# Performance work log

Hardware: AMD Instinct MI355X
Metric: run time of the kernel (lower is better)

## Reference

```python
import jax, jax.numpy as jnp
import numpy as np

N_HEAD = 16
MASK_SCALE = 10000.0  # matches torch buffer construction


def setup_inputs() -> dict:
    key = jax.random.key(0)
    k1, k2 = jax.random.split(key)
    B, T, C = 2, 2048, 1024
    x = jax.random.normal(k1, (B, T, C), dtype=jnp.float32)
    # packed q,k projection: nn.Linear(C, 2C, bias=False) -> weight [2C, C]
    W_attn = jax.random.normal(k2, (2 * C, C), dtype=jnp.float32) * 0.02
    alpha = jnp.array(1.0, dtype=jnp.float32)
    beta = jnp.array(0.1, dtype=jnp.float32)
    gamma = jnp.array(0.1, dtype=jnp.float32)
    return {"x": x, "W_attn": W_attn, "alpha": alpha, "beta": beta, "gamma": gamma}


def _shaped_attention(x, W_attn, alpha, beta, gamma):
    B, T, C = x.shape
    H = N_HEAD
    hd = C // H
    # packed projection then split into q, k (use_v=False -> v comes from x)
    qk = jnp.einsum('btc,oc->bto', x, W_attn)  # [B,T,2C]
    q, k = jnp.split(qk, 2, axis=-1)
    q = q.reshape(B, T, H, hd).transpose(0, 2, 1, 3)  # [B,H,T,hd]
    k = k.reshape(B, T, H, hd).transpose(0, 2, 1, 3)
    v = x.reshape(B, T, H, hd).transpose(0, 2, 1, 3)

    scores = jnp.einsum('bhqd,bhkd->bhqk', q, k) * (hd ** -0.5)
    tril = jnp.tril(jnp.ones((T, T), dtype=bool))
    scores = jnp.where(tril, scores, -jnp.inf)
    att = jax.nn.softmax(scores, axis=-1)  # [B,H,T,T]

    # fixed structured masks, built exactly as the torch buffers
    Id = jax.nn.softmax(jnp.eye(T, dtype=jnp.float32) * MASK_SCALE, axis=-1)
    MC = jax.nn.softmax(tril.astype(jnp.float32) * MASK_SCALE, axis=-1)

    shaped = beta * att + alpha * Id[None, None] - gamma * MC[None, None]
    y = jnp.einsum('bhqk,bhkd->bhqd', shaped, v)
    return y.transpose(0, 2, 1, 3).reshape(B, T, C)  # c_proj is Identity


def reference(x, W_attn, alpha, beta, gamma):
    return _shaped_attention(x, W_attn, alpha, beta, gamma)
```

## Files before the change

kernel.cpp:

```cpp
#include <hip/hip_runtime.h>
#include <hip/hip_bf16.h>

typedef __attribute__((ext_vector_type(8))) short bf16x8;
typedef __attribute__((ext_vector_type(4))) float f32x4;
typedef unsigned short u16;

#define B_  2
#define T_  2048
#define C_  1024
#define H_  16
#define HD_ 64

static __device__ __forceinline__ u16 f2bf(float f) {
  unsigned u = __float_as_uint(f);
  u += 0x7fffu + ((u >> 16) & 1u);
  return (u16)(u >> 16);
}

#define NW4 524288
__global__ __launch_bounds__(256) void prep(
    const float* __restrict__ X, const float* __restrict__ W,
    u16* __restrict__ Xb, u16* __restrict__ Wb,
    u16* __restrict__ Vf, float* __restrict__ SubP64)
{
  __shared__ u16 tr[64][65];
  __shared__ float cs[4][64];
  const int blk = blockIdx.x;
  const int tid = threadIdx.x;

  if (blk < 1024) {
    const int kt = blk & 31, bh = blk >> 5;
    const int b = bh >> 4, h = bh & 15;
    const int w = tid >> 6, lane = tid & 63;
    {
      const int row = tid >> 2;
      const int c0  = (tid & 3) * 16;
      const float* xp = X + ((size_t)b * T_ + kt * 64 + row) * C_ + h * 64 + c0;
      float vals[16];
#pragma unroll
      for (int q = 0; q < 4; ++q) {
        float4 v = *(const float4*)(xp + q * 4);
        vals[q * 4 + 0] = v.x; vals[q * 4 + 1] = v.y;
        vals[q * 4 + 2] = v.z; vals[q * 4 + 3] = v.w;
      }
      u16 xb[16];
#pragma unroll
      for (int i = 0; i < 16; ++i) xb[i] = f2bf(vals[i]);
      u16* xq = Xb + ((size_t)(b * T_ + kt * 64 + row)) * C_ + h * 64 + c0;
      *(bf16x8*)xq       = *(const bf16x8*)&xb[0];
      *(bf16x8*)(xq + 8) = *(const bf16x8*)&xb[8];
#pragma unroll
      for (int i = 0; i < 16; ++i) tr[row][c0 + i] = xb[i];
#pragma unroll
      for (int m = 4; m <= 32; m <<= 1)
#pragma unroll
        for (int i = 0; i < 16; ++i) vals[i] += __shfl_xor(vals[i], m);
      if (lane < 4) {
        float* dst = &cs[w][lane * 16];
#pragma unroll
        for (int q = 0; q < 4; ++q) {
          f32x4 s4 = { vals[q * 4 + 0], vals[q * 4 + 1], vals[q * 4 + 2], vals[q * 4 + 3] };
          *(f32x4*)&dst[q * 4] = s4;
        }
      }
    }
    __syncthreads();
    {
      const int quad = (lane >> 4), l16 = lane & 15;
      u16* outb = Vf + ((size_t)bh * 32 + kt) * 4096;
#pragma unroll
      for (int c = 0; c < 2; ++c) {
        u16 tmp[8];
#pragma unroll
        for (int j = 0; j < 8; ++j) tmp[j] = tr[c * 32 + quad * 8 + j][w * 16 + l16];
        *(bf16x8*)&outb[((w * 2 + c) * 64 + lane) * 8] = *(const bf16x8*)tmp;
      }
    }
    if (tid < 64)
      SubP64[(size_t)bh * 2048 + kt * 64 + tid] =
          cs[0][tid] + cs[1][tid] + cs[2][tid] + cs[3][tid];
  } else {
    int i = (blk - 1024) * 256 + tid;
    float4 v = ((const float4*)W)[i];
    ushort4 u = { f2bf(v.x), f2bf(v.y), f2bf(v.z), f2bf(v.w) };
    ((ushort4*)Wb)[i] = u;
  }
}

__global__ __launch_bounds__(256) void gemm_qk(
    const u16* __restrict__ Xb, const u16* __restrict__ Wb,
    u16* __restrict__ Qo, u16* __restrict__ Kf)
{
  __shared__ __align__(16) u16 As[128 * 64];
  __shared__ __align__(16) u16 Bs[128 * 64];

  const int tid  = threadIdx.x;
  const int w    = tid >> 6;
  const int lane = tid & 63;
  const int quad = lane >> 4;
  const int l16  = lane & 15;
  const int m0 = blockIdx.y * 128;
  const int n0 = blockIdx.x * 128;

  const int grow = w * 8 + ((lane >> 3) & 7);
  const int gcol = (lane & 7) * 8;

  f32x4 zero = {0.f, 0.f, 0.f, 0.f};
  f32x4 acc[4][4];
#pragma unroll
  for (int i = 0; i < 4; ++i)
#pragma unroll
    for (int j = 0; j < 4; ++j) acc[i][j] = zero;

  const int wr = (w >> 1) * 64, wc = (w & 1) * 64;

  for (int k0 = 0; k0 < C_; k0 += 64) {
#pragma unroll
    for (int r = 0; r < 4; ++r) {
      const u16* ga = Xb + (size_t)(m0 + grow + r * 32) * C_ + k0 + gcol;
      const u16* gb = Wb + (size_t)(n0 + grow + r * 32) * C_ + k0 + gcol;
      __builtin_amdgcn_global_load_lds(
          (const __attribute__((address_space(1))) void*)ga,
          (__attribute__((address_space(3))) void*)&As[(w * 8 + r * 32) * 64],
          16, 0, 0);
      __builtin_amdgcn_global_load_lds(
          (const __attribute__((address_space(1))) void*)gb,
          (__attribute__((address_space(3))) void*)&Bs[(w * 8 + r * 32) * 64],
          16, 0, 0);
    }
    __syncthreads();
#pragma unroll
    for (int c = 0; c < 2; ++c) {
      bf16x8 af[4], bf[4];
#pragma unroll
      for (int i = 0; i < 4; ++i)
        af[i] = *(const bf16x8*)&As[(wr + i * 16 + l16) * 64 + c * 32 + quad * 8];
#pragma unroll
      for (int j = 0; j < 4; ++j)
        bf[j] = *(const bf16x8*)&Bs[(wc + j * 16 + l16) * 64 + c * 32 + quad * 8];
#pragma unroll
      for (int i = 0; i < 4; ++i)
#pragma unroll
        for (int j = 0; j < 4; ++j)
          acc[i][j] = __builtin_amdgcn_mfma_f32_16x16x32_bf16(af[i], bf[j], acc[i][j], 0, 0, 0);
    }
    __syncthreads();
  }

#pragma unroll
  for (int i = 0; i < 4; ++i) {
    const int t_base = m0 + wr + i * 16;
    const int bidx = t_base >> 11;
    const int kt   = (t_base & 2047) >> 6;
    const int trow = (t_base & 2047) + quad * 4;
#pragma unroll
    for (int j = 0; j < 4; ++j) {
      const int n = n0 + wc + j * 16 + l16;
      if (n < C_) {
        const int hq = n >> 6, d = n & 63;
        u16* qp = Qo + (((size_t)bidx * H_ + hq) * T_ + trow) * HD_ + d;
#pragma unroll
        for (int r = 0; r < 4; ++r) qp[(size_t)r * HD_] = f2bf(0.125f * acc[i][j][r]);
      } else {
        const int nh = n - C_;
        const int hh = nh >> 6, d = nh & 63;
        u16* kp = Kf + (((((size_t)(bidx * H_ + hh) * 32 + kt) * 4 + i) * 2 + (d >> 5)) * 64
                        + ((d >> 3) & 3) * 16 + quad * 4) * 8 + (d & 7);
#pragma unroll
        for (int r = 0; r < 4; ++r) kp[(size_t)r * 8] = f2bf(acc[i][j][r]);
      }
    }
  }
}

__device__ __forceinline__ void load_kv(
    bf16x8 (&kf)[2][4], bf16x8 (&vf)[2][4],
    const u16* __restrict__ kbase, const u16* __restrict__ vbase, int lane)
{
#pragma unroll
  for (int c = 0; c < 2; ++c)
#pragma unroll
    for (int nb = 0; nb < 4; ++nb) {
      kf[c][nb] = *(const bf16x8*)&kbase[((nb * 2 + c) * 64 + lane) * 8];
      vf[c][nb] = *(const bf16x8*)&vbase[((nb * 2 + c) * 64 + lane) * 8];
    }
}

__device__ __forceinline__ void tile_compute(
    const bf16x8 (&qfrag)[2], const bf16x8 (&kf)[2][4], const bf16x8 (&vf)[2][4],
    f32x4 (&acc)[4], f32x4& accl, float (*pb)[68],
    int quad, int l16, int myrow, bool diag, bf16x8 onesf)
{
  f32x4 zero = {0.f, 0.f, 0.f, 0.f};
  f32x4 sfr[4] = {zero, zero, zero, zero};
#pragma unroll
  for (int cc = 0; cc < 2; ++cc)
#pragma unroll
    for (int nb = 0; nb < 4; ++nb)
      sfr[nb] = __builtin_amdgcn_mfma_f32_16x16x32_bf16(qfrag[cc], kf[cc][nb], sfr[nb], 0, 0, 0);

#pragma unroll
  for (int nb = 0; nb < 4; ++nb)
#pragma unroll
    for (int r = 0; r < 4; ++r) {
      float p = __expf(sfr[nb][r]);
      if (diag && (nb * 16 + l16 > myrow + r)) p = 0.f;
      pb[quad * 4 + r][nb * 16 + l16] = p;
    }

#pragma unroll
  for (int cc = 0; cc < 2; ++cc) {
    f32x4 plo = *(const f32x4*)&pb[l16][cc * 32 + quad * 8];
    f32x4 phi = *(const f32x4*)&pb[l16][cc * 32 + quad * 8 + 4];
    union { unsigned u[4]; bf16x8 v; } pk;
    __hip_bfloat162 hh;
    hh = __float22bfloat162_rn(make_float2(plo[0], plo[1])); pk.u[0] = *(unsigned*)&hh;
    hh = __float22bfloat162_rn(make_float2(plo[2], plo[3])); pk.u[1] = *(unsigned*)&hh;
    hh = __float22bfloat162_rn(make_float2(phi[0], phi[1])); pk.u[2] = *(unsigned*)&hh;
    hh = __float22bfloat162_rn(make_float2(phi[2], phi[3])); pk.u[3] = *(unsigned*)&hh;
    accl = __builtin_amdgcn_mfma_f32_16x16x32_bf16(pk.v, onesf, accl, 0, 0, 0);
#pragma unroll
    for (int nb = 0; nb < 4; ++nb)
      acc[nb] = __builtin_amdgcn_mfma_f32_16x16x32_bf16(pk.v, vf[cc][nb], acc[nb], 0, 0, 0);
  }
}

__global__ __launch_bounds__(256) void attn_kernel(
    const u16* __restrict__ Q, const u16* __restrict__ Kf, const u16* __restrict__ Vf,
    const float* __restrict__ SubP64, const float* __restrict__ X, float* __restrict__ out,
    const float* __restrict__ alphap, const float* __restrict__ betap,
    const float* __restrict__ gammap)
{
  __shared__ __align__(16) char smem[19456];

  const int tid  = threadIdx.x;
  const int w    = tid >> 6;
  const int lane = tid & 63;
  const int quad = lane >> 4;
  const int l16  = lane & 15;
  const int qt = 31 - blockIdx.y;
  const int bh = blockIdx.x;
  const int b = bh >> 4, h = bh & 15;

  const u16* kfb = Kf + (size_t)bh * T_ * HD_;
  const u16* vfb = Vf + (size_t)bh * T_ * HD_;

  bf16x8 qfrag[2];
  {
    const u16* qp = Q + ((size_t)bh * T_ + qt * 64 + w * 16 + l16) * HD_ + quad * 8;
    qfrag[0] = *(const bf16x8*)qp;
    qfrag[1] = *(const bf16x8*)(qp + 32);
  }

  bf16x8 onesf;
#pragma unroll
  for (int j = 0; j < 8; ++j) onesf[j] = (short)0x3F80;

  f32x4 zero = {0.f, 0.f, 0.f, 0.f};
  f32x4 acc[4] = {zero, zero, zero, zero};
  f32x4 accl = zero;
  const int myrow = w * 16 + quad * 4;
  float (*pb)[68] = (float(*)[68])((float*)smem + (size_t)w * 16 * 68);

  bf16x8 kA[2][4], vA[2][4], kB[2][4], vB[2][4];
  load_kv(kA, vA, kfb, vfb, lane);
  int kt = 0;
  for (;;) {
    int ktn = (kt + 1 < qt) ? kt + 1 : qt;
    load_kv(kB, vB, kfb + (size_t)ktn * 4096, vfb + (size_t)ktn * 4096, lane);
    tile_compute(qfrag, kA, vA, acc, accl, pb, quad, l16, myrow, kt == qt, onesf);
    if (kt + 1 > qt) break;
    int ktn2 = (kt + 2 < qt) ? kt + 2 : qt;
    load_kv(kA, vA, kfb + (size_t)ktn2 * 4096, vfb + (size_t)ktn2 * 4096, lane);
    tile_compute(qfrag, kB, vB, acc, accl, pb, quad, l16, myrow, kt + 1 == qt, onesf);
    kt += 2;
    if (kt > qt) break;
  }

  __syncthreads();
  float* Xt = (float*)smem;
  float* G  = (float*)(smem + 17408);
  float* GP = (float*)(smem + 18432);

  {
    const int row = tid >> 2, c0 = (tid & 3) * 16;
    const float* xp = X + ((size_t)b * T_ + qt * 64 + row) * C_ + h * 64 + c0;
#pragma unroll
    for (int q = 0; q < 4; ++q) {
      float4 v = *(const float4*)(xp + q * 4);
      Xt[row * 68 + c0 + q * 4 + 0] = v.x;
      Xt[row * 68 + c0 + q * 4 + 1] = v.y;
      Xt[row * 68 + c0 + q * 4 + 2] = v.z;
      Xt[row * 68 + c0 + q * 4 + 3] = v.w;
    }
  }
  {
    float p = 0.f;
    for (int i = w; i < qt; i += 4)
      p += SubP64[(size_t)bh * 2048 + i * 64 + lane];
    GP[w * 64 + lane] = p;
  }
  __syncthreads();
  {
    float g = 0.f;
#pragma unroll
    for (int i = 0; i < 16; ++i) g += Xt[(w * 16 + i) * 68 + lane];
    G[w * 64 + lane] = g;
  }
  __syncthreads();
  {
    const float alpha = *alphap, gamma = *gammap;
    float run = GP[lane] + GP[64 + lane] + GP[128 + lane] + GP[192 + lane];
    for (int g = 0; g < w; ++g) run += G[g * 64 + lane];
    const int tbase = qt * 64 + w * 16;
#pragma unroll
    for (int i = 0; i < 16; ++i) {
      float v = Xt[(w * 16 + i) * 68 + lane];
      run += v;
      Xt[(w * 16 + i) * 68 + lane] =
          alpha * v - gamma * run * __builtin_amdgcn_rcpf((float)(tbase + i + 1));
    }
  }
  __syncthreads();

  const float beta = *betap;
  float rl[4];
#pragma unroll
  for (int r = 0; r < 4; ++r) rl[r] = beta * __builtin_amdgcn_rcpf(accl[r]);
#pragma unroll
  for (int nb = 0; nb < 4; ++nb) {
#pragma unroll
    for (int r = 0; r < 4; ++r) {
      int t = qt * 64 + myrow + r;
      int d = nb * 16 + l16;
      out[((size_t)b * T_ + t) * C_ + h * 64 + d] =
          Xt[(myrow + r) * 68 + d] + rl[r] * acc[nb][r];
    }
  }
}

extern "C" void kernel_launch(void* const* d_in, const int* in_sizes, int n_in,
                              void* d_out, int out_size, void* d_ws, size_t ws_size,
                              hipStream_t stream) {
  const float* x      = (const float*)d_in[0];
  const float* W_attn = (const float*)d_in[1];
  const float* alphap = (const float*)d_in[2];
  const float* betap  = (const float*)d_in[3];
  const float* gammap = (const float*)d_in[4];
  float* out = (float*)d_out;

  char* ws = (char*)d_ws;
  u16*   Qb     = (u16*)(ws);
  u16*   Kfb    = (u16*)(ws + (8ull  << 20));
  u16*   Vfb    = (u16*)(ws + (16ull << 20));
  float* SubP64 = (float*)(ws + (24ull << 20));
  u16*   Xb     = (u16*)(ws + (25ull << 20));
  u16*   Wb     = (u16*)(ws + (33ull << 20));

  prep<<<3072, 256, 0, stream>>>(x, W_attn, Xb, Wb, Vfb, SubP64);
  gemm_qk<<<dim3(16, 32), 256, 0, stream>>>(Xb, Wb, Qb, Kfb);
  attn_kernel<<<dim3(32, 32), 256, 0, stream>>>(Qb, Kfb, Vfb, SubP64, x, out,
                                                alphap, betap, gammap);
}
```

Measured before the change: 151.8 us.

## Fuse fp32-to-bf16 prep into QK GEMM with register double-buffered loads

Removes the separate prep kernel. The GEMM now reads fp32 X and W directly, converts them to bf16 in registers and stores them into LDS, using register double buffering to prefetch the next k-tile. It also emits the V fragment layout and the column sums from the X tile held in LDS, on the block whose k-tile matches its head. Q is written in an MFMA fragment layout so the attention kernel can load it contiguously. This drops a launch and the bf16 round-trip through global memory. In exchange, each GEMM block redundantly re-reads and re-converts fp32 inputs, and the async global_load_lds path is gone.

```diff
diff --git a/kernel.cpp b/kernel.cpp
--- a/kernel.cpp
+++ b/kernel.cpp
@@ -16,80 +16,62 @@
   u += 0x7fffu + ((u >> 16) & 1u);
   return (u16)(u >> 16);
 }
-
-#define NW4 524288
-__global__ __launch_bounds__(256) void prep(
+static __device__ __forceinline__ unsigned pk2(float a, float b) {
+  __hip_bfloat162 hh = __float22bfloat162_rn(make_float2(a, b));
+  return *(unsigned*)&hh;
+}
+
+__device__ __forceinline__ void mfma_step(
+    const u16* As, const u16* Bs, f32x4 (&acc)[4][4],
+    int wr, int wc, int quad, int l16)
+{
+#pragma unroll
+  for (int c = 0; c < 2; ++c) {
+    bf16x8 af[4], bf[4];
+#pragma unroll
+    for (int i = 0; i < 4; ++i)
+      af[i] = *(const bf16x8*)&As[(wr + i * 16 + l16) * 64 + c * 32 + quad * 8];
+#pragma unroll
+    for (int j = 0; j < 4; ++j)
+      bf[j] = *(const bf16x8*)&Bs[(wc + j * 16 + l16) * 64 + c * 32 + quad * 8];
+#pragma unroll
+    for (int i = 0; i < 4; ++i)
+#pragma unroll
+      for (int j = 0; j < 4; ++j)
+        acc[i][j] = __builtin_amdgcn_mfma_f32_16x16x32_bf16(af[i], bf[j], acc[i][j], 0, 0, 0);
+  }
+}
+
+__device__ __forceinline__ void emit_vf(
+    const u16* As, u16* __restrict__ Vf, float* __restrict__ SubP64,
+    int bh, int kt0, int w, int lane, int quad, int l16)
+{
+#pragma unroll
+  for (int kk = 0; kk < 2; ++kk) {
+    u16* outb = Vf + ((size_t)bh * 32 + kt0 + kk) * 4096;
+    float cs = 0.f;
+#pragma unroll
+    for (int c = 0; c < 2; ++c) {
+      u16 tmp[8];
+#pragma unroll
+      for (int j = 0; j < 8; ++j) {
+        u16 v = As[(kk * 64 + c * 32 + quad * 8 + j) * 64 + w * 16 + l16];
+        tmp[j] = v;
+        cs += __uint_as_float(((unsigned)v) << 16);
+      }
+      *(bf16x8*)&outb[((w * 2 + c) * 64 + lane) * 8] = *(const bf16x8*)tmp;
+    }
+    cs += __shfl_xor(cs, 16);
+    cs += __shfl_xor(cs, 32);
+    if (quad == 0)
+      SubP64[(size_t)bh * 2048 + (kt0 + kk) * 64 + w * 16 + l16] = cs;
+  }
+}
+
+__global__ __launch_bounds__(256, 2) void gemm_fused(
     const float* __restrict__ X, const float* __restrict__ W,
-    u16* __restrict__ Xb, u16* __restrict__ Wb,
+    u16* __restrict__ Qf, u16* __restrict__ Kf,
     u16* __restrict__ Vf, float* __restrict__ SubP64)
-{
-  __shared__ u16 tr[64][65];
-  __shared__ float cs[4][64];
-  const int blk = blockIdx.x;
-  const int tid = threadIdx.x;
-
-  if (blk < 1024) {
-    const int kt = blk & 31, bh = blk >> 5;
-    const int b = bh >> 4, h = bh & 15;
-    const int w = tid >> 6, lane = tid & 63;
-    {
-      const int row = tid >> 2;
-      const int c0  = (tid & 3) * 16;
-      const float* xp = X + ((size_t)b * T_ + kt * 64 + row) * C_ + h * 64 + c0;
-      float vals[16];
-#pragma unroll
-      for (int q = 0; q < 4; ++q) {
-        float4 v = *(const float4*)(xp + q * 4);
-        vals[q * 4 + 0] = v.x; vals[q * 4 + 1] = v.y;
-        vals[q * 4 + 2] = v.z; vals[q * 4 + 3] = v.w;
-      }
-      u16 xb[16];
-#pragma unroll
-      for (int i = 0; i < 16; ++i) xb[i] = f2bf(vals[i]);
-      u16* xq = Xb + ((size_t)(b * T_ + kt * 64 + row)) * C_ + h * 64 + c0;
-      *(bf16x8*)xq       = *(const bf16x8*)&xb[0];
-      *(bf16x8*)(xq + 8) = *(const bf16x8*)&xb[8];
-#pragma unroll
-      for (int i = 0; i < 16; ++i) tr[row][c0 + i] = xb[i];
-#pragma unroll
-      for (int m = 4; m <= 32; m <<= 1)
-#pragma unroll
-        for (int i = 0; i < 16; ++i) vals[i] += __shfl_xor(vals[i], m);
-      if (lane < 4) {
-        float* dst = &cs[w][lane * 16];
-#pragma unroll
-        for (int q = 0; q < 4; ++q) {
-          f32x4 s4 = { vals[q * 4 + 0], vals[q * 4 + 1], vals[q * 4 + 2], vals[q * 4 + 3] };
-          *(f32x4*)&dst[q * 4] = s4;
-        }
-      }
-    }
-    __syncthreads();
-    {
-      const int quad = (lane >> 4), l16 = lane & 15;
-      u16* outb = Vf + ((size_t)bh * 32 + kt) * 4096;
-#pragma unroll
-      for (int c = 0; c < 2; ++c) {
-        u16 tmp[8];
-#pragma unroll
-        for (int j = 0; j < 8; ++j) tmp[j] = tr[c * 32 + quad * 8 + j][w * 16 + l16];
-        *(bf16x8*)&outb[((w * 2 + c) * 64 + lane) * 8] = *(const bf16x8*)tmp;
-      }
-    }
-    if (tid < 64)
-      SubP64[(size_t)bh * 2048 + kt * 64 + tid] =
-          cs[0][tid] + cs[1][tid] + cs[2][tid] + cs[3][tid];
-  } else {
-    int i = (blk - 1024) * 256 + tid;
-    float4 v = ((const float4*)W)[i];
-    ushort4 u = { f2bf(v.x), f2bf(v.y), f2bf(v.z), f2bf(v.w) };
-    ((ushort4*)Wb)[i] = u;
-  }
-}
-
-__global__ __launch_bounds__(256) void gemm_qk(
-    const u16* __restrict__ Xb, const u16* __restrict__ Wb,
-    u16* __restrict__ Qo, u16* __restrict__ Kf)
 {
   __shared__ __align__(16) u16 As[128 * 64];
   __shared__ __align__(16) u16 Bs[128 * 64];
@@ -101,9 +83,11 @@
   const int l16  = lane & 15;
   const int m0 = blockIdx.y * 128;
   const int n0 = blockIdx.x * 128;
-
-  const int grow = w * 8 + ((lane >> 3) & 7);
-  const int gcol = (lane & 7) * 8;
+  const int srow = tid >> 3;
+  const int scol = (tid & 7) * 8;
+
+  const float* Xs = X + (size_t)(m0 + srow) * C_ + scol;
+  const float* Ws = W + (size_t)(n0 + srow) * C_ + scol;
 
   f32x4 zero = {0.f, 0.f, 0.f, 0.f};
   f32x4 acc[4][4];
@@ -113,58 +97,77 @@
     for (int j = 0; j < 4; ++j) acc[i][j] = zero;
 
   const int wr = (w >> 1) * 64, wc = (w & 1) * 64;
-
-  for (int k0 = 0; k0 < C_; k0 += 64) {
-#pragma unroll
-    for (int r = 0; r < 4; ++r) {
-      const u16* ga = Xb + (size_t)(m0 + grow + r * 32) * C_ + k0 + gcol;
-      const u16* gb = Wb + (size_t)(n0 + grow + r * 32) * C_ + k0 + gcol;
-      __builtin_amdgcn_global_load_lds(
-          (const __attribute__((address_space(1))) void*)ga,
-          (__attribute__((address_space(3))) void*)&As[(w * 8 + r * 32) * 64],
-          16, 0, 0);
-      __builtin_amdgcn_global_load_lds(
-          (const __attribute__((address_space(1))) void*)gb,
-          (__attribute__((address_space(3))) void*)&Bs[(w * 8 + r * 32) * 64],
-          16, 0, 0);
-    }
+  const int bidx = (int)blockIdx.y >> 4;
+  const int tloc0 = m0 & 2047;
+
+#define ISSUE(K, BA, BB)                                              \
+  {                                                                   \
+    _Pragma("unroll") for (int s = 0; s < 4; ++s) {                   \
+      const float* gx = Xs + (size_t)s * 32 * C_ + (K);               \
+      BA[s * 2]     = *(const float4*)gx;                             \
+      BA[s * 2 + 1] = *(const float4*)(gx + 4);                       \
+      const float* gw = Ws + (size_t)s * 32 * C_ + (K);               \
+      BB[s * 2]     = *(const float4*)gw;                             \
+      BB[s * 2 + 1] = *(const float4*)(gw + 4);                       \
+    }                                                                 \
+  }
+#define COMMIT(BA, BB)                                                \
+  {                                                                   \
+    _Pragma("unroll") for (int s = 0; s < 4; ++s) {                   \
+      union { unsigned u[4]; bf16x8 v; } pa, pb;                      \
+      pa.u[0] = pk2(BA[s * 2].x, BA[s * 2].y);                        \
+      pa.u[1] = pk2(BA[s * 2].z, BA[s * 2].w);                        \
+      pa.u[2] = pk2(BA[s * 2 + 1].x, BA[s * 2 + 1].y);                \
+      pa.u[3] = pk2(BA[s * 2 + 1].z, BA[s * 2 + 1].w);                \
+      pb.u[0] = pk2(BB[s * 2].x, BB[s * 2].y);                        \
+      pb.u[1] = pk2(BB[s * 2].z, BB[s * 2].w);                        \
+      pb.u[2] = pk2(BB[s * 2 + 1].x, BB[s * 2 + 1].y);                \
+      pb.u[3] = pk2(BB[s * 2 + 1].z, BB[s * 2 + 1].w);                \
+      *(bf16x8*)&As[(s * 32 + srow) * 64 + scol] = pa.v;              \
+      *(bf16x8*)&Bs[(s * 32 + srow) * 64 + scol] = pb.v;              \
+    }                                                                 \
+  }
+
+  float4 a0[8], b0[8], a1[8], b1[8];
+  ISSUE(0, a0, b0);
+  for (int it = 0; it < 16; it += 2) {
+    ISSUE((it + 1) * 64, a1, b1);
+    COMMIT(a0, b0);
     __syncthreads();
-#pragma unroll
-    for (int c = 0; c < 2; ++c) {
-      bf16x8 af[4], bf[4];
-#pragma unroll
-      for (int i = 0; i < 4; ++i)
-        af[i] = *(const bf16x8*)&As[(wr + i * 16 + l16) * 64 + c * 32 + quad * 8];
-#pragma unroll
-      for (int j = 0; j < 4; ++j)
-        bf[j] = *(const bf16x8*)&Bs[(wc + j * 16 + l16) * 64 + c * 32 + quad * 8];
-#pragma unroll
-      for (int i = 0; i < 4; ++i)
-#pragma unroll
-        for (int j = 0; j < 4; ++j)
-          acc[i][j] = __builtin_amdgcn_mfma_f32_16x16x32_bf16(af[i], bf[j], acc[i][j], 0, 0, 0);
-    }
+    mfma_step(As, Bs, acc, wr, wc, quad, l16);
+    if (it == (int)blockIdx.x)
+      emit_vf(As, Vf, SubP64, bidx * H_ + blockIdx.x, tloc0 >> 6, w, lane, quad, l16);
     __syncthreads();
-  }
+    if (it + 2 < 16) ISSUE((it + 2) * 64, a0, b0);
+    COMMIT(a1, b1);
+    __syncthreads();
+    mfma_step(As, Bs, acc, wr, wc, quad, l16);
+    if (it + 1 == (int)blockIdx.x)
+      emit_vf(As, Vf, SubP64, bidx * H_ + blockIdx.x, tloc0 >> 6, w, lane, quad, l16);
+    __syncthreads();
+  }
+#undef ISSUE
+#undef COMMIT
 
 #pragma unroll
   for (int i = 0; i < 4; ++i) {
-    const int t_base = m0 + wr + i * 16;
-    const int bidx = t_base >> 11;
-    const int kt   = (t_base & 2047) >> 6;
-    const int trow = (t_base & 2047) + quad * 4;
+    const int tloc = tloc0 + wr + i * 16;
 #pragma unroll
     for (int j = 0; j < 4; ++j) {
       const int n = n0 + wc + j * 16 + l16;
       if (n < C_) {
-        const int hq = n >> 6, d = n & 63;
-        u16* qp = Qo + (((size_t)bidx * H_ + hq) * T_ + trow) * HD_ + d;
-#pragma unroll
-        for (int r = 0; r < 4; ++r) qp[(size_t)r * HD_] = f2bf(0.125f * acc[i][j][r]);
+        const int hq = n >> 6;
+        const int d = n & 63;
+        u16* qp = Qf + ((size_t)(bidx * H_ + hq) * 128 + (tloc >> 4)) * 1024
+                  + ((size_t)((d >> 5) * 64 + ((d >> 3) & 3) * 16 + quad * 4)) * 8
+                  + (d & 7);
+#pragma unroll
+        for (int r = 0; r < 4; ++r) qp[(size_t)r * 8] = f2bf(0.125f * acc[i][j][r]);
       } else {
         const int nh = n - C_;
         const int hh = nh >> 6, d = nh & 63;
-        u16* kp = Kf + (((((size_t)(bidx * H_ + hh) * 32 + kt) * 4 + i) * 2 + (d >> 5)) * 64
+        u16* kp = Kf + (((((size_t)(bidx * H_ + hh) * 32 + (tloc >> 6)) * 4
+                          + ((tloc >> 4) & 3)) * 2 + (d >> 5)) * 64
                         + ((d >> 3) & 3) * 16 + quad * 4) * 8 + (d & 7);
 #pragma unroll
         for (int r = 0; r < 4; ++r) kp[(size_t)r * 8] = f2bf(acc[i][j][r]);
@@ -213,11 +216,10 @@
     f32x4 plo = *(const f32x4*)&pb[l16][cc * 32 + quad * 8];
     f32x4 phi = *(const f32x4*)&pb[l16][cc * 32 + quad * 8 + 4];
     union { unsigned u[4]; bf16x8 v; } pk;
-    __hip_bfloat162 hh;
-    hh = __float22bfloat162_rn(make_float2(plo[0], plo[1])); pk.u[0] = *(unsigned*)&hh;
-    hh = __float22bfloat162_rn(make_float2(plo[2], plo[3])); pk.u[1] = *(unsigned*)&hh;
-    hh = __float22bfloat162_rn(make_float2(phi[0], phi[1])); pk.u[2] = *(unsigned*)&hh;
-    hh = __float22bfloat162_rn(make_float2(phi[2], phi[3])); pk.u[3] = *(unsigned*)&hh;
+    pk.u[0] = pk2(plo[0], plo[1]);
+    pk.u[1] = pk2(plo[2], plo[3]);
+    pk.u[2] = pk2(phi[0], phi[1]);
+    pk.u[3] = pk2(phi[2], phi[3]);
     accl = __builtin_amdgcn_mfma_f32_16x16x32_bf16(pk.v, onesf, accl, 0, 0, 0);
 #pragma unroll
     for (int nb = 0; nb < 4; ++nb)
@@ -226,7 +228,7 @@
 }
 
 __global__ __launch_bounds__(256) void attn_kernel(
-    const u16* __restrict__ Q, const u16* __restrict__ Kf, const u16* __restrict__ Vf,
+    const u16* __restrict__ Qf, const u16* __restrict__ Kf, const u16* __restrict__ Vf,
     const float* __restrict__ SubP64, const float* __restrict__ X, float* __restrict__ out,
     const float* __restrict__ alphap, const float* __restrict__ betap,
     const float* __restrict__ gammap)
@@ -247,9 +249,9 @@
 
   bf16x8 qfrag[2];
   {
-    const u16* qp = Q + ((size_t)bh * T_ + qt * 64 + w * 16 + l16) * HD_ + quad * 8;
-    qfrag[0] = *(const bf16x8*)qp;
-    qfrag[1] = *(const bf16x8*)(qp + 32);
+    const u16* qp = Qf + ((size_t)bh * 128 + qt * 4 + w) * 1024;
+    qfrag[0] = *(const bf16x8*)&qp[lane * 8];
+    qfrag[1] = *(const bf16x8*)&qp[(64 + lane) * 8];
   }
 
   bf16x8 onesf;
@@ -350,15 +352,12 @@
   float* out = (float*)d_out;
 
   char* ws = (char*)d_ws;
-  u16*   Qb     = (u16*)(ws);
+  u16*   Qfb    = (u16*)(ws);
   u16*   Kfb    = (u16*)(ws + (8ull  << 20));
   u16*   Vfb    = (u16*)(ws + (16ull << 20));
   float* SubP64 = (float*)(ws + (24ull << 20));
-  u16*   Xb     = (u16*)(ws + (25ull << 20));
-  u16*   Wb     = (u16*)(ws + (33ull << 20));
-
-  prep<<<3072, 256, 0, stream>>>(x, W_attn, Xb, Wb, Vfb, SubP64);
-  gemm_qk<<<dim3(16, 32), 256, 0, stream>>>(Xb, Wb, Qb, Kfb);
-  attn_kernel<<<dim3(32, 32), 256, 0, stream>>>(Qb, Kfb, Vfb, SubP64, x, out,
+
+  gemm_fused<<<dim3(16, 32), 256, 0, stream>>>(x, W_attn, Qfb, Kfb, Vfb, SubP64);
+  attn_kernel<<<dim3(32, 32), 256, 0, stream>>>(Qfb, Kfb, Vfb, SubP64, x, out,
                                                 alphap, betap, gammap);
 }
```

Result: slower. 171.2 us (+12.8%).
